# Kernel tuning notes

Measured on AMD Instinct MI355X. Metric: run time of the kernel, lower is better.

## Reference

```python
import jax, jax.numpy as jnp
import numpy as np

N_NODES = 50000
N_EDGES = 800000
HIDDEN = 128
N_REL = 64
NUM_HEADS = 8
HEAD_DIM = HIDDEN // NUM_HEADS


def setup_inputs() -> dict:
    key = jax.random.key(0)
    ks = jax.random.split(key, 20)
    s = 0.05
    inp = {
        "x": jax.random.normal(ks[0], (N_NODES, HIDDEN), dtype=jnp.float32),
        "timestamps": jax.random.uniform(ks[1], (N_NODES,), dtype=jnp.float32),
        "src": jax.random.randint(ks[2], (N_EDGES,), 0, N_NODES),
        "dst": jax.random.randint(ks[3], (N_EDGES,), 0, N_NODES),
        "edge_type": jax.random.randint(ks[4], (N_EDGES,), 0, N_REL),
        "edge_time": jax.random.uniform(ks[5], (N_EDGES,), dtype=jnp.float32),
        # parameters (torch Linear stored as [in, out] so we use x @ W + b)
        "rel_table": jax.random.normal(ks[6], (N_REL, HIDDEN), dtype=jnp.float32) * s,
        "Wq": jax.random.normal(ks[7], (HIDDEN, HIDDEN), dtype=jnp.float32) * s,
        "bq": jnp.zeros((HIDDEN,), dtype=jnp.float32),
        "Wk": jax.random.normal(ks[8], (HIDDEN, HIDDEN), dtype=jnp.float32) * s,
        "bk": jnp.zeros((HIDDEN,), dtype=jnp.float32),
        "Wv": jax.random.normal(ks[9], (HIDDEN, HIDDEN), dtype=jnp.float32) * s,
        "bv": jnp.zeros((HIDDEN,), dtype=jnp.float32),
        "W1": jax.random.normal(ks[10], (2 * HIDDEN + 1, HIDDEN), dtype=jnp.float32) * s,
        "b1": jnp.zeros((HIDDEN,), dtype=jnp.float32),
        "W2": jax.random.normal(ks[11], (HIDDEN, 1), dtype=jnp.float32) * s,
        "b2": jnp.zeros((1,), dtype=jnp.float32),
        "time_coeff": jnp.array(1.0, dtype=jnp.float32),
    }
    return inp


def reference(x, timestamps, src, dst, edge_type, edge_time, rel_table,
              Wq, bq, Wk, bk, Wv, bv, W1, b1, W2, b2, time_coeff):
    N = x.shape[0]
    # temporal gating
    delta_t = (timestamps[dst] - edge_time) / (jnp.abs(time_coeff) + 1e-9)  # [E]
    time_mask = jax.nn.sigmoid(delta_t)[:, None]                            # [E,1]
    rel_emb = rel_table[edge_type] * time_mask                              # [E,H]
    src_emb = x[src]                                                        # [E,H]
    # dynamic edge weights: MLP([src_emb, rel_emb, time_mask]) -> sigmoid
    weight_input = jnp.concatenate([src_emb, rel_emb, time_mask], axis=-1)  # [E,2H+1]
    h = jax.nn.relu(weight_input @ W1 + b1)
    dynamic_weights = jax.nn.sigmoid(h @ W2 + b2)                           # [E,1]
    message = src_emb * rel_emb * dynamic_weights                           # [E,H]
    # multi-head edge attention keyed by dst
    q = (x[dst] @ Wq + bq).reshape(-1, NUM_HEADS, HEAD_DIM)
    k = (message @ Wk + bk).reshape(-1, NUM_HEADS, HEAD_DIM)
    v = (message @ Wv + bv).reshape(-1, NUM_HEADS, HEAD_DIM)
    scores = (q * k).sum(-1) / (HEAD_DIM ** 0.5)                            # [E,heads]
    # scatter softmax over edges grouped by dst
    seg_max = jax.ops.segment_max(scores, dst, num_segments=N)              # [N,heads]
    e = jnp.exp(scores - seg_max[dst])
    denom = jax.ops.segment_sum(e, dst, num_segments=N)
    attn = e / denom[dst]                                                   # [E,heads]
    out = jax.ops.segment_sum(v * attn[..., None], dst, num_segments=N)     # [N,heads,hd]
    return out.reshape(N, NUM_HEADS * HEAD_DIM)
```

## Files before the change

kernel.cpp:

```cpp
#include <hip/hip_runtime.h>

typedef __bf16 v8bf __attribute__((ext_vector_type(8)));
typedef __bf16 v4bf __attribute__((ext_vector_type(4)));
typedef float  v4f  __attribute__((ext_vector_type(4)));

#define MFMA16x16x32 __builtin_amdgcn_mfma_f32_16x16x32_bf16

#define HIDDEN 128
#define NHEADS 8

__global__ __launch_bounds__(256) void prep_hist(
    const float* __restrict__ rel, const float* __restrict__ W1,
    const float* __restrict__ Wk, const float* __restrict__ Wv,
    const float* __restrict__ W2, const int* __restrict__ dst,
    int* __restrict__ count,
    __bf16* __restrict__ mlppre, __bf16* __restrict__ relbf,
    __bf16* __restrict__ wswz, __bf16* __restrict__ w2bf,
    float* __restrict__ outz, int E, int hb, int nz4)
{
  const int b = blockIdx.x;
  if (b < 64) {
    __shared__ float rrow[128];
    const int j = threadIdx.x;
    if (j < 128) rrow[j] = rel[b*HIDDEN + j];
    __syncthreads();
    if (j < 128) {
      float acc = W1[256*HIDDEN + j];
      #pragma unroll 4
      for (int k=0;k<128;k++) acc += rrow[k]*W1[(128+k)*HIDDEN + j];
      mlppre[b*HIDDEN + j] = (__bf16)acc;
      relbf [b*HIDDEN + j] = (__bf16)rrow[j];
    }
  } else if (b < 80) {
    int f = (b - 64)*256 + threadIdx.x;
    if (f < 128) w2bf[f] = (__bf16)W2[f];
    if (f >= 2*8*4*64) return;
    int lane = f & 63, kk = (f>>6)&3, c = (f>>8)&7, mat = f>>11;
    const float* W = mat ? Wv : Wk;
    int qq = lane>>4, nn = lane&15;
    v8bf o;
    #pragma unroll
    for (int j=0;j<8;j++) o[j] = (__bf16)W[(kk*32 + qq*8 + j)*HIDDEN + c*16 + nn];
    *(v8bf*)(wswz + (long)f*8) = o;
  } else if (b < 80 + hb) {
    long i = (long)(b - 80)*256 + threadIdx.x;
    long e4 = i*4;
    if (e4 + 3 < E) {
      int4 d = *(const int4*)(dst + e4);
      atomicAdd(&count[d.x], 1);
      atomicAdd(&count[d.y], 1);
      atomicAdd(&count[d.z], 1);
      atomicAdd(&count[d.w], 1);
    } else {
      for (long e = e4; e < E; e++) atomicAdd(&count[dst[e]], 1);
    }
  } else {
    int idx = (b - 80 - hb)*256 + threadIdx.x;
    if (idx < nz4) ((float4*)outz)[idx] = make_float4(0.f,0.f,0.f,0.f);
  }
}

__global__ __launch_bounds__(1024) void scan_kernel(const int* __restrict__ count,
    int* __restrict__ base, int N)
{
  __shared__ int ssum[1024];
  const int t = threadIdx.x;
  const int chunk = ((N + 4095) >> 12) << 2;
  const int lo = t*chunk, hi = min(lo + chunk, N);
  int s = 0;
  int i = lo;
  for (; i + 3 < hi; i += 4) {
    int4 v = *(const int4*)(count + i);
    s += v.x + v.y + v.z + v.w;
  }
  for (; i < hi; i++) s += count[i];
  ssum[t] = s;
  __syncthreads();
  #pragma unroll
  for (int ofs = 1; ofs < 1024; ofs <<= 1) {
    int v = (t >= ofs) ? ssum[t - ofs] : 0;
    __syncthreads();
    ssum[t] += v;
    __syncthreads();
  }
  int run = (t == 0) ? 0 : ssum[t-1];
  i = lo;
  for (; i + 3 < hi; i += 4) {
    int4 c = *(const int4*)(count + i);
    int4 o;
    o.x = run; o.y = run + c.x; o.z = o.y + c.y; o.w = o.z + c.z;
    *(int4*)(base + i) = o;
    run = o.w + c.w;
  }
  for (; i < hi; i++) { base[i] = run; run += count[i]; }
}

__global__ __launch_bounds__(512) void scat_pre(
    const float* __restrict__ x, const float* __restrict__ Wq,
    const float* __restrict__ bq, const float* __restrict__ W1,
    const float* __restrict__ b1,
    const int* __restrict__ src, const int* __restrict__ dstp,
    const int* __restrict__ etyp, const float* __restrict__ etime,
    const float* __restrict__ ts, const float* __restrict__ tc,
    const int* __restrict__ base, int* __restrict__ cursor,
    int4* __restrict__ meta4,
    __bf16* __restrict__ qbf, __bf16* __restrict__ hpre, __bf16* __restrict__ xbf,
    int N, int E, int SB)
{
  __shared__ __bf16 X[32][136];
  if ((int)blockIdx.x < SB) {
    int e = blockIdx.x*512 + threadIdx.x;
    if (e < E) {
      int d = dstp[e];
      int pI = base[d] + atomicAdd(&cursor[d], 1);
      float invtc = 1.0f / (fabsf(tc[0]) + 1e-9f);
      float dt = (ts[d] - etime[e]) * invtc;
      float tm = 1.0f/(1.0f + __expf(-dt));
      meta4[pI] = make_int4(src[e], d, etyp[e], __float_as_int(tm));
    }
    return;
  }
  const int pb = blockIdx.x - SB, npb = gridDim.x - SB;
  const int tid = threadIdx.x;
  const int w = tid >> 6, l = tid & 63, qd = l >> 4, ln = l & 15;
  const int col = w*16 + ln;

  v8bf BQ[4], BH[4];
  #pragma unroll
  for (int kk=0; kk<4; kk++) {
    v8bf f, g;
    #pragma unroll
    for (int j=0;j<8;j++){
      f[j] = (__bf16)Wq[(kk*32 + qd*8 + j)*HIDDEN + col];
      g[j] = (__bf16)W1[(kk*32 + qd*8 + j)*HIDDEN + col];
    }
    BQ[kk] = f; BH[kk] = g;
  }
  const float bqv = bq[col], b1v = b1[col];

  const int s = tid >> 4, c8 = (tid & 15)*8;
  for (int n0 = pb*32; n0 < N; n0 += npb*32) {
    __syncthreads();
    int n = n0 + s;
    v8bf xv;
    if (n < N) {
      const float4* xp = (const float4*)(x + (long)n*HIDDEN + c8);
      float4 a = xp[0], b = xp[1];
      xv[0]=(__bf16)a.x; xv[1]=(__bf16)a.y; xv[2]=(__bf16)a.z; xv[3]=(__bf16)a.w;
      xv[4]=(__bf16)b.x; xv[5]=(__bf16)b.y; xv[6]=(__bf16)b.z; xv[7]=(__bf16)b.w;
      *(v8bf*)(xbf + (long)n*HIDDEN + c8) = xv;
    } else {
      #pragma unroll
      for (int j=0;j<8;j++) xv[j] = (__bf16)0.f;
    }
    *(v8bf*)&X[s][c8] = xv;
    __syncthreads();

    v4f q0={0.f,0.f,0.f,0.f}, q1={0.f,0.f,0.f,0.f};
    v4f h0={0.f,0.f,0.f,0.f}, h1={0.f,0.f,0.f,0.f};
    #pragma unroll
    for (int kk=0;kk<4;kk++) {
      v8bf a0 = *(const v8bf*)&X[ln][kk*32 + qd*8];
      v8bf a1 = *(const v8bf*)&X[16+ln][kk*32 + qd*8];
      q0 = MFMA16x16x32(a0, BQ[kk], q0, 0,0,0);
      q1 = MFMA16x16x32(a1, BQ[kk], q1, 0,0,0);
      h0 = MFMA16x16x32(a0, BH[kk], h0, 0,0,0);
      h1 = MFMA16x16x32(a1, BH[kk], h1, 0,0,0);
    }
    #pragma unroll
    for (int r=0;r<4;r++) {
      int n_o = n0 + qd*4 + r;
      if (n_o < N) {
        qbf [(long)n_o*HIDDEN + col] = (__bf16)(q0[r] + bqv);
        hpre[(long)n_o*HIDDEN + col] = (__bf16)(h0[r] + b1v);
      }
      int n2 = n0 + 16 + qd*4 + r;
      if (n2 < N) {
        qbf [(long)n2*HIDDEN + col] = (__bf16)(q1[r] + bqv);
        hpre[(long)n2*HIDDEN + col] = (__bf16)(h1[r] + b1v);
      }
    }
  }
}

__global__ __launch_bounds__(256) void dw_kernel(
    int4* __restrict__ meta4,
    const __bf16* __restrict__ hpre, const __bf16* __restrict__ mlppre,
    const __bf16* __restrict__ w2bf, const float* __restrict__ b2, int E)
{
  const int tid = threadIdx.x;
  const int wid = tid >> 6, l = tid & 63;
  const int e0 = (blockIdx.x*4 + wid)*4;
  const int ei = l >> 4, lc = l & 15;

  int4 mt = make_int4(0, -1, 0, 0);
  if (l < 4 && e0 + l < E) mt = meta4[e0 + l];
  const int srcE = __shfl(mt.x, ei);
  const int tyE  = __shfl(mt.z, ei);
  const float tm = __int_as_float(__shfl(mt.w, ei));

  const v8bf w2v = *(const v8bf*)(w2bf + lc*8);
  v8bf av = *(const v8bf*)(hpre  + (long)srcE*HIDDEN + lc*8);
  v8bf bp = *(const v8bf*)(mlppre+ (long)tyE *HIDDEN + lc*8);

  float z = 0.f;
  #pragma unroll
  for (int j=0;j<8;j++){
    float pj = (float)av[j] + tm*(float)bp[j];
    z += fmaxf(pj, 0.f)*(float)w2v[j];
  }
  z += __shfl_xor(z,1); z += __shfl_xor(z,2);
  z += __shfl_xor(z,4); z += __shfl_xor(z,8);

  if (lc == 0) {
    int e = e0 + ei;
    if (e < E) {
      float dw = 1.0f/(1.0f + __expf(-(z + b2[0])));
      ((int*)meta4)[(long)e*4 + 3] = __float_as_int(tm * dw);
    }
  }
}

__global__ __launch_bounds__(512, 4) void edge_fused5(
    const int4* __restrict__ meta4,
    const __bf16* __restrict__ xbf, const __bf16* __restrict__ qbf,
    const __bf16* __restrict__ relbf, const __bf16* __restrict__ wswz,
    const float* __restrict__ bk, const float* __restrict__ bv,
    float* __restrict__ out, float* __restrict__ denom, int E, int ntiles)
{
  __shared__ __align__(16) __bf16 MSG[2][4096];

  const int tid = threadIdx.x;
  const int wid = tid >> 6, l = tid & 63, qd = l >> 4, ln = l & 15;
  const int eIdx = wid*4 + qd;

  v8bf bkf[4], bvf[4];
  #pragma unroll
  for (int kk=0;kk<4;kk++){
    bkf[kk] = *(const v8bf*)(wswz +         wid*2048 + kk*512 + (size_t)l*8);
    bvf[kk] = *(const v8bf*)(wswz + 16384 + wid*2048 + kk*512 + (size_t)l*8);
  }
  const float bkc = bk[wid*16 + ln];
  const float bvc = bv[wid*16 + ln];

  const int g = gridDim.x;
  int t = blockIdx.x;
  if (t >= ntiles) return;

  int4 mt = make_int4(0, -1, 0, 0);
  { int e = t*32 + l; if (l < 32 && e < E) mt = meta4[e]; }
  int tn = t + g;
  int4 mtn = make_int4(0, -1, 0, 0);
  if (tn < ntiles) { int e = tn*32 + l; if (l < 32 && e < E) mtn = meta4[e]; }

  float sME = __int_as_float(__shfl(mt.w, eIdx));
  v8bf sv, rv;
  {
    int srcE = __shfl(mt.x, eIdx);
    int tyE  = __shfl(mt.z, eIdx);
    sv = *(const v8bf*)(xbf   + (long)srcE*HIDDEN + ln*8);
    rv = *(const v8bf*)(relbf + (long)tyE *HIDDEN + ln*8);
  }
  int dC[2][4];
  #pragma unroll
  for (int b=0;b<2;b++)
    #pragma unroll
    for (int r=0;r<4;r++) dC[b][r] = __shfl(mt.y, b*16 + qd*4 + r);
  float qA[2][4];
  #pragma unroll
  for (int b=0;b<2;b++)
    #pragma unroll
    for (int r=0;r<4;r++){
      int d = dC[b][r];
      qA[b][r] = (float)qbf[(long)(d<0?0:d)*HIDDEN + wid*16 + ln];
    }

  int p = 0;
  while (true) {
    const int d_m = mt.y;

    int dprev = __shfl(d_m, (l>0)?(l-1):0);
    int flag = (l < 32) && ((l==0) || (d_m != dprev));
    unsigned long long segmask = __ballot(flag);

    const int t2 = tn + g;
    int4 mt2 = make_int4(0, -1, 0, 0);
    if (t2 < ntiles) { int e = t2*32 + l; if (l < 32 && e < E) mt2 = meta4[e]; }

    const float sMN = __int_as_float(__shfl(mtn.w, eIdx));
    const int srcN = __shfl(mtn.x, eIdx);
    const int tyN  = __shfl(mtn.z, eIdx);
    int dN[2][4];
    #pragma unroll
    for (int b=0;b<2;b++)
      #pragma unroll
      for (int r=0;r<4;r++) dN[b][r] = __shfl(mtn.y, b*16 + qd*4 + r);

    {
      char* wbase = (char*)&MSG[p][0] + eIdx*256;
      const int sw = (eIdx & 7) << 4;
      v8bf m;
      #pragma unroll
      for (int j=0;j<8;j++) m[j] = (__bf16)((float)sv[j]*(float)rv[j]*sME);
      *(v8bf*)(wbase + ((ln*16) ^ sw)) = m;
    }

    sv = *(const v8bf*)(xbf   + (long)srcN*HIDDEN + ln*8);
    rv = *(const v8bf*)(relbf + (long)tyN *HIDDEN + ln*8);

    float qB[2][4];
    #pragma unroll
    for (int b=0;b<2;b++)
      #pragma unroll
      for (int r=0;r<4;r++){
        int d = dN[b][r];
        qB[b][r] = (float)qbf[(long)(d<0?0:d)*HIDDEN + wid*16 + ln];
      }

    asm volatile("s_waitcnt lgkmcnt(0)" ::: "memory");
    __builtin_amdgcn_s_barrier();
    __builtin_amdgcn_sched_barrier(0);

    const char* rb = (const char*)&MSG[p][0];
    v4f aK[2], aV[2];
    __builtin_amdgcn_s_setprio(1);
    #pragma unroll
    for (int b=0;b<2;b++){
      const int rrow = b*16 + ln;
      const char* abase = rb + rrow*256;
      const int asw = (rrow & 7) << 4;
      v4f k_ = {0.f,0.f,0.f,0.f}, v_ = {0.f,0.f,0.f,0.f};
      #pragma unroll
      for (int kk=0;kk<4;kk++){
        v8bf a = *(const v8bf*)(abase + ((kk*64 + qd*16) ^ asw));
        k_ = MFMA16x16x32(a, bkf[kk], k_, 0,0,0);
        v_ = MFMA16x16x32(a, bvf[kk], v_, 0,0,0);
      }
      aK[b] = k_; aV[b] = v_;
    }
    __builtin_amdgcn_s_setprio(0);

    float sc[2][4];
    #pragma unroll
    for (int b=0;b<2;b++)
      #pragma unroll
      for (int r=0;r<4;r++) sc[b][r] = (aK[b][r] + bkc)*qA[b][r];
    #pragma unroll
    for (int m=1;m<16;m<<=1){
      #pragma unroll
      for (int b=0;b<2;b++)
        #pragma unroll
        for (int r=0;r<4;r++) sc[b][r] += __shfl_xor(sc[b][r], m);
    }
    float ee[2][4], wv[2][4];
    #pragma unroll
    for (int b=0;b<2;b++)
      #pragma unroll
      for (int r=0;r<4;r++){
        float e_ = __expf(sc[b][r]*0.25f);
        ee[b][r] = e_;
        wv[b][r] = e_*(aV[b][r] + bvc);
      }

    unsigned long long mm = segmask;
    while (mm){
      int s0 = __ffsll((long long)mm) - 1;
      mm &= mm - 1;
      int s1 = mm ? (__ffsll((long long)mm) - 1) : 32;
      int dseg = __shfl(d_m, s0);
      if (dseg < 0) continue;
      float a0 = 0.f, dn0 = 0.f;
      #pragma unroll
      for (int b=0;b<2;b++)
        #pragma unroll
        for (int r=0;r<4;r++){
          int rw = b*16 + qd*4 + r;
          bool in = (rw >= s0) && (rw < s1);
          a0  += in ? wv[b][r] : 0.f;
          dn0 += in ? ee[b][r] : 0.f;
        }
      a0  += __shfl_xor(a0,16);  a0  += __shfl_xor(a0,32);
      dn0 += __shfl_xor(dn0,16); dn0 += __shfl_xor(dn0,32);
      if (l < 16) atomicAdd(&out[(long)dseg*HIDDEN + wid*16 + ln], a0);
      if (l == 0) atomicAdd(&denom[(long)dseg*NHEADS + wid], dn0);
    }

    if (tn >= ntiles) break;
    t = tn; tn = t2; mt = mtn; mtn = mt2; sME = sMN;
    #pragma unroll
    for (int b=0;b<2;b++)
      #pragma unroll
      for (int r=0;r<4;r++){
        dC[b][r] = dN[b][r];
        qA[b][r] = qB[b][r];
      }
    p ^= 1;
  }
}

__global__ __launch_bounds__(512) void q_kernel(const float* __restrict__ x,
    const float* __restrict__ Wq, const float* __restrict__ bq,
    float* __restrict__ q, int N)
{
  __shared__ __bf16 X[32][136];
  const int tid = threadIdx.x;
  const int w = tid >> 6, l = tid & 63, qd = l >> 4, ln = l & 15;
  const int col = w*16 + ln;
  v8bf B[4];
  #pragma unroll
  for (int kk=0; kk<4; kk++) {
    v8bf f;
    #pragma unroll
    for (int j=0;j<8;j++) f[j] = (__bf16)Wq[(kk*32 + qd*8 + j)*HIDDEN + col];
    B[kk] = f;
  }
  const float bqv = bq[col];
  const int s = tid >> 4, c8 = (tid & 15)*8;
  for (int n0 = blockIdx.x*32; n0 < N; n0 += gridDim.x*32) {
    __syncthreads();
    int n = n0 + s;
    v8bf xv;
    if (n < N) {
      const float4* xp = (const float4*)(x + (long)n*HIDDEN + c8);
      float4 a = xp[0], b = xp[1];
      xv[0]=(__bf16)a.x; xv[1]=(__bf16)a.y; xv[2]=(__bf16)a.z; xv[3]=(__bf16)a.w;
      xv[4]=(__bf16)b.x; xv[5]=(__bf16)b.y; xv[6]=(__bf16)b.z; xv[7]=(__bf16)b.w;
    } else {
      #pragma unroll
      for (int j=0;j<8;j++) xv[j] = (__bf16)0.f;
    }
    *(v8bf*)&X[s][c8] = xv;
    __syncthreads();
    v4f acc0 = {0.f,0.f,0.f,0.f}, acc1 = {0.f,0.f,0.f,0.f};
    #pragma unroll
    for (int kk=0;kk<4;kk++) {
      v8bf a0 = *(const v8bf*)&X[ln][kk*32 + qd*8];
      v8bf a1 = *(const v8bf*)&X[16+ln][kk*32 + qd*8];
      acc0 = MFMA16x16x32(a0, B[kk], acc0, 0,0,0);
      acc1 = MFMA16x16x32(a1, B[kk], acc1, 0,0,0);
    }
    #pragma unroll
    for (int r=0;r<4;r++) {
      int n_o = n0 + qd*4 + r;
      if (n_o < N) q[(long)n_o*HIDDEN + col] = acc0[r] + bqv;
      int n_o2 = n0 + 16 + qd*4 + r;
      if (n_o2 < N) q[(long)n_o2*HIDDEN + col] = acc1[r] + bqv;
    }
  }
}

__global__ __launch_bounds__(512) void edge_atomic(
    const float* __restrict__ x, const float* __restrict__ ts,
    const int* __restrict__ src, const int* __restrict__ dst,
    const int* __restrict__ etyp, const float* __restrict__ etime,
    const float* __restrict__ rel,
    const float* __restrict__ Wk, const float* __restrict__ bk,
    const float* __restrict__ Wv, const float* __restrict__ bv,
    const float* __restrict__ W1, const float* __restrict__ b1,
    const float* __restrict__ W2, const float* __restrict__ b2,
    const float* __restrict__ tc,
    const float* __restrict__ qws, float* __restrict__ denom,
    float* __restrict__ out, int E)
{
  __shared__ __bf16 A[32][264];
  __shared__ __bf16 A2[32][136];
  __shared__ float sW2[128], sb1[128], sw1r[128], sbk[128], sbv[128];
  __shared__ float stm[32], sdw[32];
  __shared__ int   ssrc[32], sdst[32], styp[32];
  __shared__ float dwpart[8][32];
  const int tid = threadIdx.x;
  const int w = tid >> 6, l = tid & 63, qd = l >> 4, ln = l & 15;
  const int col = w*16 + ln;
  v8bf B1[8], BK[4], BV[4];
  #pragma unroll
  for (int kk=0;kk<8;kk++){ v8bf f;
    #pragma unroll
    for (int j=0;j<8;j++) f[j] = (__bf16)W1[(kk*32+qd*8+j)*HIDDEN + col];
    B1[kk]=f; }
  #pragma unroll
  for (int kk=0;kk<4;kk++){ v8bf f,g;
    #pragma unroll
    for (int j=0;j<8;j++){ f[j] = (__bf16)Wk[(kk*32+qd*8+j)*HIDDEN + col];
                           g[j] = (__bf16)Wv[(kk*32+qd*8+j)*HIDDEN + col]; }
    BK[kk]=f; BV[kk]=g; }
  if (tid < 128) {
    sW2[tid]=W2[tid]; sb1[tid]=b1[tid]; sw1r[tid]=W1[256*HIDDEN+tid];
    sbk[tid]=bk[tid]; sbv[tid]=bv[tid];
  }
  const float b2v = b2[0];
  const float invtc = 1.0f / (fabsf(tc[0]) + 1e-9f);
  const int s = tid >> 4, c8 = (tid & 15)*8;
  const int ntiles = (E + 31) >> 5;
  for (int t = blockIdx.x; t < ntiles; t += gridDim.x) {
    const int e0 = t*32;
    __syncthreads();
    if (tid < 32) {
      int e = e0 + tid;
      if (e < E) {
        int d = dst[e];
        ssrc[tid]=src[e]; sdst[tid]=d; styp[tid]=etyp[e];
        float dt = (ts[d] - etime[e]) * invtc;
        stm[tid] = 1.0f/(1.0f+expf(-dt));
      } else { ssrc[tid]=0; sdst[tid]=0; styp[tid]=0; stm[tid]=0.f; }
    }
    __syncthreads();
    {
      const float tmv = stm[s];
      const float4* xp = (const float4*)(x + (long)ssrc[s]*HIDDEN + c8);
      float4 a = xp[0], b = xp[1];
      const float4* rp = (const float4*)(rel + (long)styp[s]*HIDDEN + c8);
      float4 ra = rp[0], rb = rp[1];
      v8bf sv, rv;
      sv[0]=(__bf16)a.x; sv[1]=(__bf16)a.y; sv[2]=(__bf16)a.z; sv[3]=(__bf16)a.w;
      sv[4]=(__bf16)b.x; sv[5]=(__bf16)b.y; sv[6]=(__bf16)b.z; sv[7]=(__bf16)b.w;
      rv[0]=(__bf16)(ra.x*tmv); rv[1]=(__bf16)(ra.y*tmv);
      rv[2]=(__bf16)(ra.z*tmv); rv[3]=(__bf16)(ra.w*tmv);
      rv[4]=(__bf16)(rb.x*tmv); rv[5]=(__bf16)(rb.y*tmv);
      rv[6]=(__bf16)(rb.z*tmv); rv[7]=(__bf16)(rb.w*tmv);
      *(v8bf*)&A[s][c8] = sv;
      *(v8bf*)&A[s][128 + c8] = rv;
    }
    __syncthreads();
    v4f acc0={0.f,0.f,0.f,0.f}, acc1={0.f,0.f,0.f,0.f};
    #pragma unroll
    for (int kk=0;kk<8;kk++){
      v8bf a0 = *(const v8bf*)&A[ln][kk*32 + qd*8];
      v8bf a1 = *(const v8bf*)&A[16+ln][kk*32 + qd*8];
      acc0 = MFMA16x16x32(a0, B1[kk], acc0, 0,0,0);
      acc1 = MFMA16x16x32(a1, B1[kk], acc1, 0,0,0);
    }
    float part[8];
    {
      const float w1rj = sw1r[col], b1j = sb1[col], w2j = sW2[col];
      #pragma unroll
      for (int r=0;r<4;r++){
        int i0 = qd*4 + r, i1 = 16 + qd*4 + r;
        part[r]   = fmaxf(acc0[r] + stm[i0]*w1rj + b1j, 0.f)*w2j;
        part[4+r] = fmaxf(acc1[r] + stm[i1]*w1rj + b1j, 0.f)*w2j;
      }
    }
    #pragma unroll
    for (int m=1;m<16;m<<=1){
      #pragma unroll
      for (int i=0;i<8;i++) part[i] += __shfl_xor(part[i], m, 16);
    }
    if (ln == 0){
      #pragma unroll
      for (int r=0;r<4;r++){ dwpart[w][qd*4+r]=part[r]; dwpart[w][16+qd*4+r]=part[4+r]; }
    }
    __syncthreads();
    if (tid < 32){
      float z = b2v;
      #pragma unroll
      for (int ww=0;ww<8;ww++) z += dwpart[ww][tid];
      sdw[tid] = 1.0f/(1.0f+expf(-z));
    }
    __syncthreads();
    {
      const float dwv = sdw[s];
      v8bf mv;
      #pragma unroll
      for (int i=0;i<8;i++)
        mv[i] = (__bf16)((float)A[s][c8+i]*(float)A[s][128+c8+i]*dwv);
      *(v8bf*)&A2[s][c8] = mv;
    }
    __syncthreads();
    v4f k0={0.f,0.f,0.f,0.f}, k1={0.f,0.f,0.f,0.f};
    v4f v0={0.f,0.f,0.f,0.f}, v1={0.f,0.f,0.f,0.f};
    #pragma unroll
    for (int kk=0;kk<4;kk++){
      v8bf a0 = *(const v8bf*)&A2[ln][kk*32 + qd*8];
      v8bf a1 = *(const v8bf*)&A2[16+ln][kk*32 + qd*8];
      k0 = MFMA16x16x32(a0, BK[kk], k0, 0,0,0);
      k1 = MFMA16x16x32(a1, BK[kk], k1, 0,0,0);
      v0 = MFMA16x16x32(a0, BV[kk], v0, 0,0,0);
      v1 = MFMA16x16x32(a1, BV[kk], v1, 0,0,0);
    }
    float sc[8];
    const float bkj = sbk[col], bvj = sbv[col];
    #pragma unroll
    for (int r=0;r<4;r++){
      int i0 = qd*4 + r, i1 = 16 + qd*4 + r;
      sc[r]   = (k0[r]+bkj)*qws[(long)sdst[i0]*HIDDEN + col];
      sc[4+r] = (k1[r]+bkj)*qws[(long)sdst[i1]*HIDDEN + col];
    }
    #pragma unroll
    for (int m=1;m<16;m<<=1){
      #pragma unroll
      for (int i=0;i<8;i++) sc[i] += __shfl_xor(sc[i], m, 16);
    }
    float ee[8];
    #pragma unroll
    for (int i=0;i<8;i++) ee[i] = expf(sc[i]*0.25f);
    if (ln == 0){
      #pragma unroll
      for (int r=0;r<4;r++){
        int i0 = qd*4 + r, i1 = 16 + qd*4 + r;
        if (e0+i0 < E) atomicAdd(&denom[(long)sdst[i0]*NHEADS + w], ee[r]);
        if (e0+i1 < E) atomicAdd(&denom[(long)sdst[i1]*NHEADS + w], ee[4+r]);
      }
    }
    #pragma unroll
    for (int r=0;r<4;r++){
      int i0 = qd*4 + r, i1 = 16 + qd*4 + r;
      if (e0+i0 < E) atomicAdd(&out[(long)sdst[i0]*HIDDEN + col], ee[r]*(v0[r]+bvj));
      if (e0+i1 < E) atomicAdd(&out[(long)sdst[i1]*HIDDEN + col], ee[4+r]*(v1[r]+bvj));
    }
  }
}

__global__ void fin_kernel(float* __restrict__ out, const float* __restrict__ denom, int N)
{
  int idx = blockIdx.x*blockDim.x + threadIdx.x;
  int total = N*32;
  if (idx < total){
    int n = idx >> 5;
    int h = (idx & 31) >> 2;
    float d = denom[n*8 + h];
    float inv = d > 0.f ? 1.0f/d : 0.f;
    float4* p = (float4*)out + idx;
    float4 v = *p;
    v.x*=inv; v.y*=inv; v.z*=inv; v.w*=inv;
    *p = v;
  }
}

static inline size_t align256(size_t v){ return (v + 255) & ~(size_t)255; }

extern "C" void kernel_launch(void* const* d_in, const int* in_sizes, int n_in,
                              void* d_out, int out_size, void* d_ws, size_t ws_size,
                              hipStream_t stream)
{
  const float* x      = (const float*)d_in[0];
  const float* ts     = (const float*)d_in[1];
  const int*   src    = (const int*)d_in[2];
  const int*   dstp   = (const int*)d_in[3];
  const int*   etyp   = (const int*)d_in[4];
  const float* etime  = (const float*)d_in[5];
  const float* rel    = (const float*)d_in[6];
  const float* Wq     = (const float*)d_in[7];
  const float* bq     = (const float*)d_in[8];
  const float* Wk     = (const float*)d_in[9];
  const float* bk     = (const float*)d_in[10];
  const float* Wv     = (const float*)d_in[11];
  const float* bv     = (const float*)d_in[12];
  const float* W1     = (const float*)d_in[13];
  const float* b1     = (const float*)d_in[14];
  const float* W2     = (const float*)d_in[15];
  const float* b2     = (const float*)d_in[16];
  const float* tc     = (const float*)d_in[17];
  float* out = (float*)d_out;

  const int N = in_sizes[0] / HIDDEN;
  const int E = in_sizes[2];

  char* ws = (char*)d_ws;
  size_t off = 0;
  __bf16* qbf    = (__bf16*)(ws + off); off += align256((size_t)N*HIDDEN*2);
  __bf16* hpre   = (__bf16*)(ws + off); off += align256((size_t)N*HIDDEN*2);
  __bf16* xbf    = (__bf16*)(ws + off); off += align256((size_t)N*HIDDEN*2);
  __bf16* relbf  = (__bf16*)(ws + off); off += align256((size_t)64*HIDDEN*2);
  __bf16* mlppre = (__bf16*)(ws + off); off += align256((size_t)64*HIDDEN*2);
  __bf16* w2bf   = (__bf16*)(ws + off); off += align256((size_t)HIDDEN*2);
  __bf16* wswz   = (__bf16*)(ws + off); off += align256((size_t)4096*8*2);
  size_t zoff = off;
  int*    countp = (int*)(ws + off);    off += align256((size_t)N*4);
  int*    cursor = (int*)(ws + off);    off += align256((size_t)N*4);
  float*  denom  = (float*)(ws + off);  off += align256((size_t)N*NHEADS*4);
  size_t zlen = off - zoff;
  int4*   meta4  = (int4*)(ws + off);   off += align256((size_t)E*16);
  int*    basep  = (int*)(ws + off);    off += align256((size_t)N*4);
  const size_t needed_fast = off;

  if (ws_size >= needed_fast) {
    hipMemsetAsync(ws + zoff, 0, zlen, stream);

    const int hb = (E + 1023)/1024;
    const int nz4 = N*32;
    const int zb = (nz4 + 255)/256;
    prep_hist<<<80 + hb + zb, 256, 0, stream>>>(rel, W1, Wk, Wv, W2, dstp, countp,
        mlppre, relbf, wswz, w2bf, out, E, hb, nz4);
    scan_kernel<<<1, 1024, 0, stream>>>(countp, basep, N);
    const int SB = (E + 511)/512;
    scat_pre<<<SB + 1024, 512, 0, stream>>>(x, Wq, bq, W1, b1,
        src, dstp, etyp, etime, ts, tc, basep, cursor, meta4,
        qbf, hpre, xbf, N, E, SB);
    dw_kernel<<<(E + 15)/16, 256, 0, stream>>>(meta4, hpre, mlppre, w2bf, b2, E);

    const int ntiles = (E + 31) >> 5;
    edge_fused5<<<1024, 512, 0, stream>>>(meta4,
        xbf, qbf, relbf, wswz, bk, bv, out, denom, E, ntiles);
    fin_kernel<<<(N*32 + 255)/256, 256, 0, stream>>>(out, denom, N);
  } else {
    float* qws    = (float*)ws;
    float* denom2 = (float*)(ws + align256((size_t)N*HIDDEN*4));
    hipMemsetAsync(out,    0, (size_t)N*HIDDEN*4, stream);
    hipMemsetAsync(denom2, 0, (size_t)N*NHEADS*4, stream);
    q_kernel<<<512, 512, 0, stream>>>(x, Wq, bq, qws, N);
    edge_atomic<<<512, 512, 0, stream>>>(x, ts, src, dstp, etyp, etime, rel,
        Wk, bk, Wv, bv, W1, b1, W2, b2, tc, qws, denom2, out, E);
    fin_kernel<<<(N*32 + 255)/256, 256, 0, stream>>>(out, denom2, N);
  }
}
```

Before: 480.4 us.

## Fuse node projections into prep kernel and merge scatter with dynamic-weight computation

The per-node Q and MLP-pre projections move from the scatter kernel into the prep kernel (histogram, zeroing, weight swizzle), with block sizes widened to 512. The edge scatter and the dynamic-weight MLP are merged into one kernel that computes the time mask and weight in unsorted edge order and writes the final meta record directly to its CSR slot. This removes one launch and one full read/rewrite pass over meta4. In exchange the hpre gathers happen in random edge order, and the scatter kernel now reads edge arrays with only 4 of 64 lanes active.

```diff
diff --git a/kernel.cpp b/kernel.cpp
--- a/kernel.cpp
+++ b/kernel.cpp
@@ -9,15 +9,20 @@
 #define HIDDEN 128
 #define NHEADS 8
 
-__global__ __launch_bounds__(256) void prep_hist(
+__global__ __launch_bounds__(512) void prep_all(
     const float* __restrict__ rel, const float* __restrict__ W1,
     const float* __restrict__ Wk, const float* __restrict__ Wv,
     const float* __restrict__ W2, const int* __restrict__ dst,
     int* __restrict__ count,
     __bf16* __restrict__ mlppre, __bf16* __restrict__ relbf,
     __bf16* __restrict__ wswz, __bf16* __restrict__ w2bf,
-    float* __restrict__ outz, int E, int hb, int nz4)
-{
+    float* __restrict__ outz,
+    const float* __restrict__ x, const float* __restrict__ Wq,
+    const float* __restrict__ bq, const float* __restrict__ b1,
+    __bf16* __restrict__ qbf, __bf16* __restrict__ hpre, __bf16* __restrict__ xbf,
+    int N, int E, int hb, int zb, int nz4)
+{
+  __shared__ __bf16 X[32][136];
   const int b = blockIdx.x;
   if (b < 64) {
     __shared__ float rrow[128];
@@ -31,8 +36,10 @@
       mlppre[b*HIDDEN + j] = (__bf16)acc;
       relbf [b*HIDDEN + j] = (__bf16)rrow[j];
     }
-  } else if (b < 80) {
-    int f = (b - 64)*256 + threadIdx.x;
+    return;
+  }
+  if (b < 72) {
+    int f = (b - 64)*512 + threadIdx.x;
     if (f < 128) w2bf[f] = (__bf16)W2[f];
     if (f >= 2*8*4*64) return;
     int lane = f & 63, kk = (f>>6)&3, c = (f>>8)&7, mat = f>>11;
@@ -42,8 +49,10 @@
     #pragma unroll
     for (int j=0;j<8;j++) o[j] = (__bf16)W[(kk*32 + qq*8 + j)*HIDDEN + c*16 + nn];
     *(v8bf*)(wswz + (long)f*8) = o;
-  } else if (b < 80 + hb) {
-    long i = (long)(b - 80)*256 + threadIdx.x;
+    return;
+  }
+  if (b < 72 + hb) {
+    long i = (long)(b - 72)*512 + threadIdx.x;
     long e4 = i*4;
     if (e4 + 3 < E) {
       int4 d = *(const int4*)(dst + e4);
@@ -54,9 +63,73 @@
     } else {
       for (long e = e4; e < E; e++) atomicAdd(&count[dst[e]], 1);
     }
-  } else {
-    int idx = (b - 80 - hb)*256 + threadIdx.x;
+    return;
+  }
+  if (b < 72 + hb + zb) {
+    int idx = (b - 72 - hb)*512 + threadIdx.x;
     if (idx < nz4) ((float4*)outz)[idx] = make_float4(0.f,0.f,0.f,0.f);
+    return;
+  }
+  const int pb = b - (72 + hb + zb), npb = gridDim.x - (72 + hb + zb);
+  const int tid = threadIdx.x;
+  const int w = tid >> 6, l = tid & 63, qd = l >> 4, ln = l & 15;
+  const int col = w*16 + ln;
+
+  v8bf BQ[4], BH[4];
+  #pragma unroll
+  for (int kk=0; kk<4; kk++) {
+    v8bf f, g;
+    #pragma unroll
+    for (int j=0;j<8;j++){
+      f[j] = (__bf16)Wq[(kk*32 + qd*8 + j)*HIDDEN + col];
+      g[j] = (__bf16)W1[(kk*32 + qd*8 + j)*HIDDEN + col];
+    }
+    BQ[kk] = f; BH[kk] = g;
+  }
+  const float bqv = bq[col], b1v = b1[col];
+
+  const int s = tid >> 4, c8 = (tid & 15)*8;
+  for (int n0 = pb*32; n0 < N; n0 += npb*32) {
+    __syncthreads();
+    int n = n0 + s;
+    v8bf xv;
+    if (n < N) {
+      const float4* xp = (const float4*)(x + (long)n*HIDDEN + c8);
+      float4 a = xp[0], b2_ = xp[1];
+      xv[0]=(__bf16)a.x; xv[1]=(__bf16)a.y; xv[2]=(__bf16)a.z; xv[3]=(__bf16)a.w;
+      xv[4]=(__bf16)b2_.x; xv[5]=(__bf16)b2_.y; xv[6]=(__bf16)b2_.z; xv[7]=(__bf16)b2_.w;
+      *(v8bf*)(xbf + (long)n*HIDDEN + c8) = xv;
+    } else {
+      #pragma unroll
+      for (int j=0;j<8;j++) xv[j] = (__bf16)0.f;
+    }
+    *(v8bf*)&X[s][c8] = xv;
+    __syncthreads();
+
+    v4f q0={0.f,0.f,0.f,0.f}, q1={0.f,0.f,0.f,0.f};
+    v4f h0={0.f,0.f,0.f,0.f}, h1={0.f,0.f,0.f,0.f};
+    #pragma unroll
+    for (int kk=0;kk<4;kk++) {
+      v8bf a0 = *(const v8bf*)&X[ln][kk*32 + qd*8];
+      v8bf a1 = *(const v8bf*)&X[16+ln][kk*32 + qd*8];
+      q0 = MFMA16x16x32(a0, BQ[kk], q0, 0,0,0);
+      q1 = MFMA16x16x32(a1, BQ[kk], q1, 0,0,0);
+      h0 = MFMA16x16x32(a0, BH[kk], h0, 0,0,0);
+      h1 = MFMA16x16x32(a1, BH[kk], h1, 0,0,0);
+    }
+    #pragma unroll
+    for (int r=0;r<4;r++) {
+      int n_o = n0 + qd*4 + r;
+      if (n_o < N) {
+        qbf [(long)n_o*HIDDEN + col] = (__bf16)(q0[r] + bqv);
+        hpre[(long)n_o*HIDDEN + col] = (__bf16)(h0[r] + b1v);
+      }
+      int n2 = n0 + 16 + qd*4 + r;
+      if (n2 < N) {
+        qbf [(long)n2*HIDDEN + col] = (__bf16)(q1[r] + bqv);
+        hpre[(long)n2*HIDDEN + col] = (__bf16)(h1[r] + b1v);
+      }
+    }
   }
 }
 
@@ -95,113 +168,38 @@
   for (; i < hi; i++) { base[i] = run; run += count[i]; }
 }
 
-__global__ __launch_bounds__(512) void scat_pre(
-    const float* __restrict__ x, const float* __restrict__ Wq,
-    const float* __restrict__ bq, const float* __restrict__ W1,
-    const float* __restrict__ b1,
+__global__ __launch_bounds__(512) void scat_dw(
     const int* __restrict__ src, const int* __restrict__ dstp,
     const int* __restrict__ etyp, const float* __restrict__ etime,
     const float* __restrict__ ts, const float* __restrict__ tc,
+    const __bf16* __restrict__ hpre, const __bf16* __restrict__ mlppre,
+    const __bf16* __restrict__ w2bf, const float* __restrict__ b2,
     const int* __restrict__ base, int* __restrict__ cursor,
-    int4* __restrict__ meta4,
-    __bf16* __restrict__ qbf, __bf16* __restrict__ hpre, __bf16* __restrict__ xbf,
-    int N, int E, int SB)
-{
-  __shared__ __bf16 X[32][136];
-  if ((int)blockIdx.x < SB) {
-    int e = blockIdx.x*512 + threadIdx.x;
-    if (e < E) {
-      int d = dstp[e];
-      int pI = base[d] + atomicAdd(&cursor[d], 1);
-      float invtc = 1.0f / (fabsf(tc[0]) + 1e-9f);
-      float dt = (ts[d] - etime[e]) * invtc;
-      float tm = 1.0f/(1.0f + __expf(-dt));
-      meta4[pI] = make_int4(src[e], d, etyp[e], __float_as_int(tm));
-    }
-    return;
-  }
-  const int pb = blockIdx.x - SB, npb = gridDim.x - SB;
-  const int tid = threadIdx.x;
-  const int w = tid >> 6, l = tid & 63, qd = l >> 4, ln = l & 15;
-  const int col = w*16 + ln;
-
-  v8bf BQ[4], BH[4];
-  #pragma unroll
-  for (int kk=0; kk<4; kk++) {
-    v8bf f, g;
-    #pragma unroll
-    for (int j=0;j<8;j++){
-      f[j] = (__bf16)Wq[(kk*32 + qd*8 + j)*HIDDEN + col];
-      g[j] = (__bf16)W1[(kk*32 + qd*8 + j)*HIDDEN + col];
-    }
-    BQ[kk] = f; BH[kk] = g;
-  }
-  const float bqv = bq[col], b1v = b1[col];
-
-  const int s = tid >> 4, c8 = (tid & 15)*8;
-  for (int n0 = pb*32; n0 < N; n0 += npb*32) {
-    __syncthreads();
-    int n = n0 + s;
-    v8bf xv;
-    if (n < N) {
-      const float4* xp = (const float4*)(x + (long)n*HIDDEN + c8);
-      float4 a = xp[0], b = xp[1];
-      xv[0]=(__bf16)a.x; xv[1]=(__bf16)a.y; xv[2]=(__bf16)a.z; xv[3]=(__bf16)a.w;
-      xv[4]=(__bf16)b.x; xv[5]=(__bf16)b.y; xv[6]=(__bf16)b.z; xv[7]=(__bf16)b.w;
-      *(v8bf*)(xbf + (long)n*HIDDEN + c8) = xv;
-    } else {
-      #pragma unroll
-      for (int j=0;j<8;j++) xv[j] = (__bf16)0.f;
-    }
-    *(v8bf*)&X[s][c8] = xv;
-    __syncthreads();
-
-    v4f q0={0.f,0.f,0.f,0.f}, q1={0.f,0.f,0.f,0.f};
-    v4f h0={0.f,0.f,0.f,0.f}, h1={0.f,0.f,0.f,0.f};
-    #pragma unroll
-    for (int kk=0;kk<4;kk++) {
-      v8bf a0 = *(const v8bf*)&X[ln][kk*32 + qd*8];
-      v8bf a1 = *(const v8bf*)&X[16+ln][kk*32 + qd*8];
-      q0 = MFMA16x16x32(a0, BQ[kk], q0, 0,0,0);
-      q1 = MFMA16x16x32(a1, BQ[kk], q1, 0,0,0);
-      h0 = MFMA16x16x32(a0, BH[kk], h0, 0,0,0);
-      h1 = MFMA16x16x32(a1, BH[kk], h1, 0,0,0);
-    }
-    #pragma unroll
-    for (int r=0;r<4;r++) {
-      int n_o = n0 + qd*4 + r;
-      if (n_o < N) {
-        qbf [(long)n_o*HIDDEN + col] = (__bf16)(q0[r] + bqv);
-        hpre[(long)n_o*HIDDEN + col] = (__bf16)(h0[r] + b1v);
-      }
-      int n2 = n0 + 16 + qd*4 + r;
-      if (n2 < N) {
-        qbf [(long)n2*HIDDEN + col] = (__bf16)(q1[r] + bqv);
-        hpre[(long)n2*HIDDEN + col] = (__bf16)(h1[r] + b1v);
-      }
-    }
-  }
-}
-
-__global__ __launch_bounds__(256) void dw_kernel(
-    int4* __restrict__ meta4,
-    const __bf16* __restrict__ hpre, const __bf16* __restrict__ mlppre,
-    const __bf16* __restrict__ w2bf, const float* __restrict__ b2, int E)
+    int4* __restrict__ meta4, int E)
 {
   const int tid = threadIdx.x;
   const int wid = tid >> 6, l = tid & 63;
-  const int e0 = (blockIdx.x*4 + wid)*4;
+  const long e0 = ((long)blockIdx.x*8 + wid)*4;
   const int ei = l >> 4, lc = l & 15;
 
-  int4 mt = make_int4(0, -1, 0, 0);
-  if (l < 4 && e0 + l < E) mt = meta4[e0 + l];
-  const int srcE = __shfl(mt.x, ei);
-  const int tyE  = __shfl(mt.z, ei);
-  const float tm = __int_as_float(__shfl(mt.w, ei));
+  int s_=0, d_=0, ty_=0; float et_=0.f, tsd_=0.f;
+  if (l < 4 && e0 + l < E) {
+    long e = e0 + l;
+    s_ = src[e]; d_ = dstp[e]; ty_ = etyp[e]; et_ = etime[e]; tsd_ = ts[d_];
+  }
+  const int sE  = __shfl(s_, ei);
+  const int dE  = __shfl(d_, ei);
+  const int tyE = __shfl(ty_, ei);
+  const float etE  = __shfl(et_, ei);
+  const float tsdE = __shfl(tsd_, ei);
+
+  const float invtc = 1.0f / (fabsf(tc[0]) + 1e-9f);
+  const float dt = (tsdE - etE) * invtc;
+  const float tm = 1.0f/(1.0f + __expf(-dt));
 
   const v8bf w2v = *(const v8bf*)(w2bf + lc*8);
-  v8bf av = *(const v8bf*)(hpre  + (long)srcE*HIDDEN + lc*8);
-  v8bf bp = *(const v8bf*)(mlppre+ (long)tyE *HIDDEN + lc*8);
+  v8bf av = *(const v8bf*)(hpre  + (long)sE *HIDDEN + lc*8);
+  v8bf bp = *(const v8bf*)(mlppre+ (long)tyE*HIDDEN + lc*8);
 
   float z = 0.f;
   #pragma unroll
@@ -212,12 +210,10 @@
   z += __shfl_xor(z,1); z += __shfl_xor(z,2);
   z += __shfl_xor(z,4); z += __shfl_xor(z,8);
 
-  if (lc == 0) {
-    int e = e0 + ei;
-    if (e < E) {
-      float dw = 1.0f/(1.0f + __expf(-(z + b2[0])));
-      ((int*)meta4)[(long)e*4 + 3] = __float_as_int(tm * dw);
-    }
+  if (lc == 0 && e0 + ei < E) {
+    float dw = 1.0f/(1.0f + __expf(-(z + b2[0])));
+    int p = base[dE] + atomicAdd(&cursor[dE], 1);
+    meta4[p] = make_int4(sE, dE, tyE, __float_as_int(tm * dw));
   }
 }
 
@@ -675,17 +671,15 @@
   if (ws_size >= needed_fast) {
     hipMemsetAsync(ws + zoff, 0, zlen, stream);
 
-    const int hb = (E + 1023)/1024;
+    const int hb = (E + 2047)/2048;
     const int nz4 = N*32;
-    const int zb = (nz4 + 255)/256;
-    prep_hist<<<80 + hb + zb, 256, 0, stream>>>(rel, W1, Wk, Wv, W2, dstp, countp,
-        mlppre, relbf, wswz, w2bf, out, E, hb, nz4);
+    const int zb = (nz4 + 511)/512;
+    prep_all<<<72 + hb + zb + 1024, 512, 0, stream>>>(rel, W1, Wk, Wv, W2,
+        dstp, countp, mlppre, relbf, wswz, w2bf, out,
+        x, Wq, bq, b1, qbf, hpre, xbf, N, E, hb, zb, nz4);
     scan_kernel<<<1, 1024, 0, stream>>>(countp, basep, N);
-    const int SB = (E + 511)/512;
-    scat_pre<<<SB + 1024, 512, 0, stream>>>(x, Wq, bq, W1, b1,
-        src, dstp, etyp, etime, ts, tc, basep, cursor, meta4,
-        qbf, hpre, xbf, N, E, SB);
-    dw_kernel<<<(E + 15)/16, 256, 0, stream>>>(meta4, hpre, mlppre, w2bf, b2, E);
+    scat_dw<<<(E + 31)/32, 512, 0, stream>>>(src, dstp, etyp, etime, ts, tc,
+        hpre, mlppre, w2bf, b2, basep, cursor, meta4, E);
 
     const int ntiles = (E + 31) >> 5;
     edge_fused5<<<1024, 512, 0, stream>>>(meta4,
```

Result: faster. 462.5 us (-3.7%).
